# Kernel tuning notes

Hardware: AMD Instinct MI355X
Metric: run time of the kernel (lower is better)

## Reference

```python
import jax, jax.numpy as jnp
import numpy as np

H, T, E = 8, 2048, 512


def setup_inputs() -> dict:
    key = jax.random.key(0)
    ks = jax.random.split(key, 11)
    s_e = 1.0 / np.sqrt(E)
    s_f = 1.0 / np.sqrt(H * T)
    return {
        "x": jax.random.normal(ks[0], (T, E), jnp.float32),
        "y": jax.random.normal(ks[1], (T, E), jnp.float32),
        "z": jax.random.normal(ks[2], (T, E), jnp.float32),
        "Wq": jax.random.normal(ks[3], (H, E, E), jnp.float32) * s_e,
        "bq": jax.random.normal(ks[4], (H, E), jnp.float32) * s_e,
        "Wk": jax.random.normal(ks[5], (H, E, E), jnp.float32) * s_e,
        "bk": jax.random.normal(ks[6], (H, E), jnp.float32) * s_e,
        "Wv": jax.random.normal(ks[7], (H, E, E), jnp.float32) * s_e,
        "bv": jax.random.normal(ks[8], (H, E), jnp.float32) * s_e,
        "Wf": jax.random.normal(ks[9], (T, H * T), jnp.float32) * s_f,
        "bf": jax.random.normal(ks[10], (T,), jnp.float32) * s_f,
    }


def reference(x, y, z, Wq, bq, Wk, bk, Wv, bv, Wf, bf):
    # Per-head projections: torch Linear is x @ W.T + b, W is [out,in]
    q = jnp.einsum("se,hfe->hsf", x, Wq) + bq[:, None, :]  # [H,T,E]
    k = jnp.einsum("se,hfe->hsf", y, Wk) + bk[:, None, :]
    v = jnp.einsum("se,hfe->hsf", z, Wv) + bv[:, None, :]
    # Scores scaled by sqrt(num query rows) = sqrt(T), as in the source
    scores = jnp.einsum("hsf,htf->hst", q, k) / jnp.sqrt(jnp.asarray(T, x.dtype))
    att = jax.nn.softmax(scores, axis=-1)
    heads_out = jnp.einsum("hst,htf->hsf", att, v)  # [H,T,E]
    concat = heads_out.reshape(H * T, E)  # cat along dim 0
    # finalLinear applied to concat.T: [E, H*T] @ Wf.T -> [E, T], then transpose
    final = (concat.T @ Wf.T + bf).T  # [T, E]
    residual = final + z
    # Manual per-row LayerNorm: (x - mean) / sqrt(std^2 + 1e-4), population std
    mean = jnp.mean(residual, axis=1, keepdims=True)
    var = jnp.var(residual, axis=1, keepdims=True)
    return (residual - mean) / jnp.sqrt(var + 1e-4)
```

## Files before the change

### kernel.cpp

```cpp
#include <hip/hip_runtime.h>
#include <hip/hip_bf16.h>
#include <cstdint>


#define HH 8
#define TT 2048
#define EE 512
#define HT (HH * TT)

typedef __bf16 bf16_t;
typedef __attribute__((ext_vector_type(8))) __bf16 bf16x8;
typedef __attribute__((ext_vector_type(4))) float f32x4;

__device__ __forceinline__ void stage_half(const bf16_t* __restrict__ g, bf16_t* l) {
  __builtin_amdgcn_global_load_lds(
      (const __attribute__((address_space(1))) unsigned int*)g,
      (__attribute__((address_space(3))) unsigned int*)l, 16, 0, 0);
}
__device__ __forceinline__ void stage_half(const float* __restrict__ g, bf16_t* l) {
  float4 u = ((const float4*)g)[0];
  float4 v = ((const float4*)g)[1];
  bf16x8 o;
  o[0] = (__bf16)u.x; o[1] = (__bf16)u.y; o[2] = (__bf16)u.z; o[3] = (__bf16)u.w;
  o[4] = (__bf16)v.x; o[5] = (__bf16)v.y; o[6] = (__bf16)v.z; o[7] = (__bf16)v.w;
  *(bf16x8*)l = o;
}

template <typename CT, bool ATOMIC>
__device__ __forceinline__ void store_c(CT* p, float v) {
  if constexpr (ATOMIC) atomicAdd((float*)p, v);
  else *p = (CT)v;
}

template <typename AT, typename CT, bool ATOMIC>
__global__ __launch_bounds__(256) void mfma_gemm_nt(
    const AT* __restrict__ A, const bf16_t* __restrict__ B, CT* __restrict__ C,
    const float* __restrict__ bias_m, const float* __restrict__ bias_n,
    int K, int lda, int ldb, int ldc,
    int64_t sA, int64_t sB, int64_t sC, int64_t sBM, int64_t sBN) {
  const int z = blockIdx.z;
  A += z * sA;
  B += z * sB;
  C += z * sC;
  if (bias_m) bias_m += z * sBM;
  if (bias_n) bias_n += z * sBN;

  const int m0 = blockIdx.x * 128;
  const int n0 = blockIdx.y * 128;
  const int tid = threadIdx.x;

  __shared__ bf16_t sAb[128 * 32];
  __shared__ bf16_t sBb[128 * 32];

  const int srow = tid >> 2;
  const int scol = (tid & 3) * 8;
  const AT* a0 = A + (int64_t)(m0 + srow) * lda + scol;
  const AT* a1 = a0 + (int64_t)64 * lda;
  const bf16_t* b0 = B + (int64_t)(n0 + srow) * ldb + scol;
  const bf16_t* b1 = b0 + (int64_t)64 * ldb;
  bf16_t* la0 = sAb + tid * 8;
  bf16_t* la1 = sAb + 2048 + tid * 8;
  bf16_t* lb0 = sBb + tid * 8;
  bf16_t* lb1 = sBb + 2048 + tid * 8;

  const int wave = tid >> 6;
  const int lane = tid & 63;
  const int wm = (wave >> 1) * 64;
  const int wn = (wave & 1) * 64;
  const int fr = lane & 15;
  const int qd = lane >> 4;

  f32x4 acc[4][4];
#pragma unroll
  for (int i = 0; i < 4; i++)
#pragma unroll
    for (int j = 0; j < 4; j++) acc[i][j] = (f32x4){0.f, 0.f, 0.f, 0.f};

  for (int kt = 0; kt < K; kt += 32) {
    __syncthreads();
    stage_half(a0 + kt, la0);
    stage_half(a1 + kt, la1);
    stage_half(b0 + kt, lb0);
    stage_half(b1 + kt, lb1);
    __syncthreads();

    bf16x8 af[4], bf_[4];
#pragma unroll
    for (int i = 0; i < 4; i++)
      af[i] = *(const bf16x8*)&sAb[(wm + i * 16 + fr) * 32 + qd * 8];
#pragma unroll
    for (int j = 0; j < 4; j++)
      bf_[j] = *(const bf16x8*)&sBb[(wn + j * 16 + fr) * 32 + qd * 8];
#pragma unroll
    for (int i = 0; i < 4; i++)
#pragma unroll
      for (int j = 0; j < 4; j++)
        acc[i][j] = __builtin_amdgcn_mfma_f32_16x16x32_bf16(af[i], bf_[j], acc[i][j], 0, 0, 0);
  }

#pragma unroll
  for (int i = 0; i < 4; i++) {
    const int row0 = m0 + wm + i * 16 + qd * 4;
#pragma unroll
    for (int j = 0; j < 4; j++) {
      const int col = n0 + wn + j * 16 + fr;
      const float bn = bias_n ? bias_n[col] : 0.f;
#pragma unroll
      for (int r = 0; r < 4; r++) {
        const float bm = bias_m ? bias_m[row0 + r] : 0.f;
        store_c<CT, ATOMIC>(&C[(int64_t)(row0 + r) * ldc + col], acc[i][j][r] + bn + bm);
      }
    }
  }
}

__global__ __launch_bounds__(256) void cvt_bf16(const float* __restrict__ s,
                                                bf16_t* __restrict__ d) {
  const int64_t i = ((int64_t)blockIdx.x * 256 + threadIdx.x) * 8;
  float4 u = ((const float4*)(s + i))[0];
  float4 v = ((const float4*)(s + i))[1];
  bf16x8 o;
  o[0] = (__bf16)u.x; o[1] = (__bf16)u.y; o[2] = (__bf16)u.z; o[3] = (__bf16)u.w;
  o[4] = (__bf16)v.x; o[5] = (__bf16)v.y; o[6] = (__bf16)v.z; o[7] = (__bf16)v.w;
  *(bf16x8*)(d + i) = o;
}

__global__ __launch_bounds__(256) void softmax_rows(bf16_t* __restrict__ S) {
  const float scale = 0.022097086912079608f;
  bf16_t* p = S + (int64_t)blockIdx.x * TT;
  const int tid = threadIdx.x;
  float v[8];
  float mx = -1e30f;
#pragma unroll
  for (int i = 0; i < 8; i++) {
    v[i] = (float)p[tid + i * 256] * scale;
    mx = fmaxf(mx, v[i]);
  }
#pragma unroll
  for (int o = 32; o > 0; o >>= 1) mx = fmaxf(mx, __shfl_xor(mx, o));
  __shared__ float redm[4], reds[4];
  if ((tid & 63) == 0) redm[tid >> 6] = mx;
  __syncthreads();
  mx = fmaxf(fmaxf(redm[0], redm[1]), fmaxf(redm[2], redm[3]));
  float sum = 0.f;
#pragma unroll
  for (int i = 0; i < 8; i++) {
    v[i] = __expf(v[i] - mx);
    sum += v[i];
  }
#pragma unroll
  for (int o = 32; o > 0; o >>= 1) sum += __shfl_xor(sum, o);
  if ((tid & 63) == 0) reds[tid >> 6] = sum;
  __syncthreads();
  sum = reds[0] + reds[1] + reds[2] + reds[3];
  const float inv = 1.0f / sum;
#pragma unroll
  for (int i = 0; i < 8; i++) p[tid + i * 256] = (__bf16)(v[i] * inv);
}

__global__ __launch_bounds__(256) void ln_res(const float* __restrict__ F,
                                              const float* __restrict__ Z,
                                              const float* __restrict__ BF,
                                              float* __restrict__ O) {
  const int row = blockIdx.x;
  const float* f = F + (int64_t)row * EE;
  const float* z = Z + (int64_t)row * EE;
  float* o = O + (int64_t)row * EE;
  const float bft = BF[row];
  const int tid = threadIdx.x;
  const float a = f[tid] + bft + z[tid];
  const float b = f[tid + 256] + bft + z[tid + 256];
  float s = a + b, ss = a * a + b * b;
#pragma unroll
  for (int w = 32; w > 0; w >>= 1) {
    s += __shfl_xor(s, w);
    ss += __shfl_xor(ss, w);
  }
  __shared__ float rs[4], rss[4];
  if ((tid & 63) == 0) {
    rs[tid >> 6] = s;
    rss[tid >> 6] = ss;
  }
  __syncthreads();
  s = rs[0] + rs[1] + rs[2] + rs[3];
  ss = rss[0] + rss[1] + rss[2] + rss[3];
  const float mean = s * (1.0f / EE);
  const float var = ss * (1.0f / EE) - mean * mean;
  const float inv = rsqrtf(var + 1e-4f);
  o[tid] = (a - mean) * inv;
  o[tid + 256] = (b - mean) * inv;
}

extern "C" void kernel_launch(void* const* d_in, const int* in_sizes, int n_in,
                              void* d_out, int out_size, void* d_ws, size_t ws_size,
                              hipStream_t stream) {
  const float* x = (const float*)d_in[0];
  const float* y = (const float*)d_in[1];
  const float* z = (const float*)d_in[2];
  const float* Wq = (const float*)d_in[3];
  const float* bq = (const float*)d_in[4];
  const float* Wk = (const float*)d_in[5];
  const float* bk = (const float*)d_in[6];
  const float* Wv = (const float*)d_in[7];
  const float* bv = (const float*)d_in[8];
  const float* Wf = (const float*)d_in[9];
  const float* bfb = (const float*)d_in[10];
  float* out = (float*)d_out;

  const size_t MB = 1ull << 20;
  char* p = (char*)d_ws;

  const int64_t nTE = (int64_t)TT * EE;
  const int64_t nW = (int64_t)HH * EE * EE;

  if (ws_size >= 151 * MB) {
    bf16_t* xb = (bf16_t*)(p + 0 * MB);
    bf16_t* yb = (bf16_t*)(p + 2 * MB);
    bf16_t* zb = (bf16_t*)(p + 4 * MB);
    bf16_t* Wqb = (bf16_t*)(p + 6 * MB);
    bf16_t* Wkb = (bf16_t*)(p + 10 * MB);
    bf16_t* Wvb = (bf16_t*)(p + 14 * MB);
    bf16_t* q = (bf16_t*)(p + 18 * MB);
    bf16_t* k = (bf16_t*)(p + 34 * MB);
    bf16_t* vT = (bf16_t*)(p + 50 * MB);
    bf16_t* att = (bf16_t*)(p + 66 * MB);
    bf16_t* hoT = (bf16_t*)(p + 130 * MB);
    float* fin = (float*)(p + 146 * MB);

    cvt_bf16<<<nTE / 2048, 256, 0, stream>>>(x, xb);
    cvt_bf16<<<nTE / 2048, 256, 0, stream>>>(y, yb);
    cvt_bf16<<<nTE / 2048, 256, 0, stream>>>(z, zb);
    cvt_bf16<<<nW / 2048, 256, 0, stream>>>(Wq, Wqb);
    cvt_bf16<<<nW / 2048, 256, 0, stream>>>(Wk, Wkb);
    cvt_bf16<<<nW / 2048, 256, 0, stream>>>(Wv, Wvb);

    mfma_gemm_nt<bf16_t, bf16_t, false><<<dim3(16, 4, 8), 256, 0, stream>>>(
        xb, Wqb, q, nullptr, bq, EE, EE, EE, EE, 0, (int64_t)EE * EE, (int64_t)TT * EE, 0, EE);
    mfma_gemm_nt<bf16_t, bf16_t, false><<<dim3(16, 4, 8), 256, 0, stream>>>(
        yb, Wkb, k, nullptr, bk, EE, EE, EE, EE, 0, (int64_t)EE * EE, (int64_t)TT * EE, 0, EE);
    mfma_gemm_nt<bf16_t, bf16_t, false><<<dim3(4, 16, 8), 256, 0, stream>>>(
        Wvb, zb, vT, bv, nullptr, EE, EE, EE, TT, (int64_t)EE * EE, 0, (int64_t)EE * TT, EE, 0);
    mfma_gemm_nt<bf16_t, bf16_t, false><<<dim3(16, 16, 8), 256, 0, stream>>>(
        q, k, att, nullptr, nullptr, EE, EE, EE, TT, (int64_t)TT * EE, (int64_t)TT * EE,
        (int64_t)TT * TT, 0, 0);
    softmax_rows<<<HH * TT, 256, 0, stream>>>(att);
    mfma_gemm_nt<bf16_t, bf16_t, false><<<dim3(4, 16, 8), 256, 0, stream>>>(
        vT, att, hoT, nullptr, nullptr, TT, TT, TT, HT, (int64_t)EE * TT, (int64_t)TT * TT,
        (int64_t)TT, 0, 0);
    hipMemsetAsync(fin, 0, (size_t)TT * EE * 4, stream);
    mfma_gemm_nt<float, float, true><<<dim3(16, 4, 8), 256, 0, stream>>>(
        Wf, hoT, fin, nullptr, nullptr, HT / 8, HT, HT, EE, HT / 8, HT / 8, 0, 0, 0);
    ln_res<<<TT, 256, 0, stream>>>(fin, z, bfb, out);
  } else {
    bf16_t* xb = (bf16_t*)(p + 0 * MB);
    bf16_t* yb = (bf16_t*)(p + 2 * MB);
    bf16_t* zb = (bf16_t*)(p + 4 * MB);
    bf16_t* Wqb = (bf16_t*)(p + 6 * MB);
    bf16_t* Wkb = (bf16_t*)(p + 10 * MB);
    bf16_t* Wvb = (bf16_t*)(p + 14 * MB);
    bf16_t* qh = (bf16_t*)(p + 18 * MB);
    bf16_t* kh = (bf16_t*)(p + 20 * MB);
    bf16_t* vTh = (bf16_t*)(p + 22 * MB);
    bf16_t* att = (bf16_t*)(p + 24 * MB);
    bf16_t* hoT = (bf16_t*)(p + 32 * MB);
    float* fin = (float*)(p + 48 * MB);

    cvt_bf16<<<nTE / 2048, 256, 0, stream>>>(x, xb);
    cvt_bf16<<<nTE / 2048, 256, 0, stream>>>(y, yb);
    cvt_bf16<<<nTE / 2048, 256, 0, stream>>>(z, zb);
    cvt_bf16<<<nW / 2048, 256, 0, stream>>>(Wq, Wqb);
    cvt_bf16<<<nW / 2048, 256, 0, stream>>>(Wk, Wkb);
    cvt_bf16<<<nW / 2048, 256, 0, stream>>>(Wv, Wvb);

    for (int h = 0; h < HH; h++) {
      const bf16_t* Wq_h = Wqb + (int64_t)h * EE * EE;
      const bf16_t* Wk_h = Wkb + (int64_t)h * EE * EE;
      const bf16_t* Wv_h = Wvb + (int64_t)h * EE * EE;
      mfma_gemm_nt<bf16_t, bf16_t, false><<<dim3(16, 4, 1), 256, 0, stream>>>(
          xb, Wq_h, qh, nullptr, bq + h * EE, EE, EE, EE, EE, 0, 0, 0, 0, 0);
      mfma_gemm_nt<bf16_t, bf16_t, false><<<dim3(16, 4, 1), 256, 0, stream>>>(
          yb, Wk_h, kh, nullptr, bk + h * EE, EE, EE, EE, EE, 0, 0, 0, 0, 0);
      mfma_gemm_nt<bf16_t, bf16_t, false><<<dim3(4, 16, 1), 256, 0, stream>>>(
          Wv_h, zb, vTh, bv + h * EE, nullptr, EE, EE, EE, TT, 0, 0, 0, 0, 0);
      mfma_gemm_nt<bf16_t, bf16_t, false><<<dim3(16, 16, 1), 256, 0, stream>>>(
          qh, kh, att, nullptr, nullptr, EE, EE, EE, TT, 0, 0, 0, 0, 0);
      softmax_rows<<<TT, 256, 0, stream>>>(att);
      mfma_gemm_nt<bf16_t, bf16_t, false><<<dim3(4, 16, 1), 256, 0, stream>>>(
          vTh, att, hoT + (int64_t)h * TT, nullptr, nullptr, TT, TT, TT, HT, 0, 0, 0, 0, 0);
    }
    hipMemsetAsync(fin, 0, (size_t)TT * EE * 4, stream);
    mfma_gemm_nt<float, float, true><<<dim3(16, 4, 8), 256, 0, stream>>>(
        Wf, hoT, fin, nullptr, nullptr, HT / 8, HT, HT, EE, HT / 8, HT / 8, 0, 0, 0);
    ln_res<<<TT, 256, 0, stream>>>(fin, z, bfb, out);
  }
}
```

Before: 528.6 us.

## Add split-K for PV and final GEMMs, fp32 register prefetch, vectorized softmax

The GEMM kernel gains a templated split-K dimension (NZK) folded into blockIdx.z; bias is added only by the first K slice. It also gains register prefetch of the next fp32 tile, so global loads overlap with the MFMA loop. When the workspace is large enough, a new path splits the attention-times-V GEMM in two, accumulating into a zero-initialised fp32 hoT buffer with atomics. The final Wf GEMM is split 16 ways on every path, and softmax loads and stores rows with contiguous 16-byte vectors. The aim is more parallelism and better latency hiding, at the cost of extra memsets, atomic traffic and a larger fp32 intermediate.

```diff
diff --git a/kernel.cpp b/kernel.cpp
--- a/kernel.cpp
+++ b/kernel.cpp
@@ -1,6 +1,7 @@
 #include <hip/hip_runtime.h>
 #include <hip/hip_bf16.h>
 #include <cstdint>
+#include <type_traits>
 
 
 #define HH 8
@@ -12,17 +13,21 @@
 typedef __attribute__((ext_vector_type(8))) __bf16 bf16x8;
 typedef __attribute__((ext_vector_type(4))) float f32x4;
 
-__device__ __forceinline__ void stage_half(const bf16_t* __restrict__ g, bf16_t* l) {
+__device__ __forceinline__ void stage_lds(const bf16_t* __restrict__ g, bf16_t* l) {
   __builtin_amdgcn_global_load_lds(
       (const __attribute__((address_space(1))) unsigned int*)g,
       (__attribute__((address_space(3))) unsigned int*)l, 16, 0, 0);
 }
-__device__ __forceinline__ void stage_half(const float* __restrict__ g, bf16_t* l) {
-  float4 u = ((const float4*)g)[0];
-  float4 v = ((const float4*)g)[1];
+
+struct PF { float4 lo, hi; };
+__device__ __forceinline__ void pf_load(const float* __restrict__ g, PF& r) {
+  r.lo = ((const float4*)g)[0];
+  r.hi = ((const float4*)g)[1];
+}
+__device__ __forceinline__ void pf_store(bf16_t* l, const PF& r) {
   bf16x8 o;
-  o[0] = (__bf16)u.x; o[1] = (__bf16)u.y; o[2] = (__bf16)u.z; o[3] = (__bf16)u.w;
-  o[4] = (__bf16)v.x; o[5] = (__bf16)v.y; o[6] = (__bf16)v.z; o[7] = (__bf16)v.w;
+  o[0] = (__bf16)r.lo.x; o[1] = (__bf16)r.lo.y; o[2] = (__bf16)r.lo.z; o[3] = (__bf16)r.lo.w;
+  o[4] = (__bf16)r.hi.x; o[5] = (__bf16)r.hi.y; o[6] = (__bf16)r.hi.z; o[7] = (__bf16)r.hi.w;
   *(bf16x8*)l = o;
 }
 
@@ -32,18 +37,23 @@
   else *p = (CT)v;
 }
 
-template <typename AT, typename CT, bool ATOMIC>
+template <typename AT, typename BT, typename CT, bool ATOMIC, int NZK>
 __global__ __launch_bounds__(256) void mfma_gemm_nt(
-    const AT* __restrict__ A, const bf16_t* __restrict__ B, CT* __restrict__ C,
+    const AT* __restrict__ A, const BT* __restrict__ B, CT* __restrict__ C,
     const float* __restrict__ bias_m, const float* __restrict__ bias_n,
     int K, int lda, int ldb, int ldc,
-    int64_t sA, int64_t sB, int64_t sC, int64_t sBM, int64_t sBN) {
-  const int z = blockIdx.z;
-  A += z * sA;
-  B += z * sB;
-  C += z * sC;
-  if (bias_m) bias_m += z * sBM;
-  if (bias_n) bias_n += z * sBN;
+    int64_t sAh, int64_t sAk, int64_t sBh, int64_t sBk, int64_t sCh,
+    int64_t sBMh, int64_t sBNh) {
+  constexpr bool A_F32 = std::is_same<AT, float>::value;
+  constexpr bool B_F32 = std::is_same<BT, float>::value;
+  const int zh = blockIdx.z / NZK;
+  const int zk = blockIdx.z % NZK;
+  A += zh * sAh + zk * sAk;
+  B += zh * sBh + zk * sBk;
+  C += zh * sCh;
+  const bool do_bias = (zk == 0);
+  if (bias_m) bias_m += zh * sBMh;
+  if (bias_n) bias_n += zh * sBNh;
 
   const int m0 = blockIdx.x * 128;
   const int n0 = blockIdx.y * 128;
@@ -56,8 +66,8 @@
   const int scol = (tid & 3) * 8;
   const AT* a0 = A + (int64_t)(m0 + srow) * lda + scol;
   const AT* a1 = a0 + (int64_t)64 * lda;
-  const bf16_t* b0 = B + (int64_t)(n0 + srow) * ldb + scol;
-  const bf16_t* b1 = b0 + (int64_t)64 * ldb;
+  const BT* b0 = B + (int64_t)(n0 + srow) * ldb + scol;
+  const BT* b1 = b0 + (int64_t)64 * ldb;
   bf16_t* la0 = sAb + tid * 8;
   bf16_t* la1 = sAb + 2048 + tid * 8;
   bf16_t* lb0 = sBb + tid * 8;
@@ -76,26 +86,50 @@
 #pragma unroll
     for (int j = 0; j < 4; j++) acc[i][j] = (f32x4){0.f, 0.f, 0.f, 0.f};
 
+  PF pa0, pa1, pb0, pb1;
+  if constexpr (A_F32) { pf_load((const float*)a0, pa0); pf_load((const float*)a1, pa1); }
+  if constexpr (B_F32) { pf_load((const float*)b0, pb0); pf_load((const float*)b1, pb1); }
+
   for (int kt = 0; kt < K; kt += 32) {
     __syncthreads();
-    stage_half(a0 + kt, la0);
-    stage_half(a1 + kt, la1);
-    stage_half(b0 + kt, lb0);
-    stage_half(b1 + kt, lb1);
+    if constexpr (A_F32) {
+      pf_store(la0, pa0);
+      pf_store(la1, pa1);
+    } else {
+      stage_lds((const bf16_t*)a0 + kt, la0);
+      stage_lds((const bf16_t*)a1 + kt, la1);
+    }
+    if constexpr (B_F32) {
+      pf_store(lb0, pb0);
+      pf_store(lb1, pb1);
+    } else {
+      stage_lds((const bf16_t*)b0 + kt, lb0);
+      stage_lds((const bf16_t*)b1 + kt, lb1);
+    }
+    if (kt + 32 < K) {
+      if constexpr (A_F32) {
+        pf_load((const float*)a0 + kt + 32, pa0);
+        pf_load((const float*)a1 + kt + 32, pa1);
+      }
+      if constexpr (B_F32) {
+        pf_load((const float*)b0 + kt + 32, pb0);
+        pf_load((const float*)b1 + kt + 32, pb1);
+      }
+    }
     __syncthreads();
 
-    bf16x8 af[4], bf_[4];
+    bf16x8 af[4], bfr[4];
 #pragma unroll
     for (int i = 0; i < 4; i++)
       af[i] = *(const bf16x8*)&sAb[(wm + i * 16 + fr) * 32 + qd * 8];
 #pragma unroll
     for (int j = 0; j < 4; j++)
-      bf_[j] = *(const bf16x8*)&sBb[(wn + j * 16 + fr) * 32 + qd * 8];
+      bfr[j] = *(const bf16x8*)&sBb[(wn + j * 16 + fr) * 32 + qd * 8];
 #pragma unroll
     for (int i = 0; i < 4; i++)
 #pragma unroll
       for (int j = 0; j < 4; j++)
-        acc[i][j] = __builtin_amdgcn_mfma_f32_16x16x32_bf16(af[i], bf_[j], acc[i][j], 0, 0, 0);
+        acc[i][j] = __builtin_amdgcn_mfma_f32_16x16x32_bf16(af[i], bfr[j], acc[i][j], 0, 0, 0);
   }
 
 #pragma unroll
@@ -104,10 +138,10 @@
 #pragma unroll
     for (int j = 0; j < 4; j++) {
       const int col = n0 + wn + j * 16 + fr;
-      const float bn = bias_n ? bias_n[col] : 0.f;
+      const float bn = (bias_n && do_bias) ? bias_n[col] : 0.f;
 #pragma unroll
       for (int r = 0; r < 4; r++) {
-        const float bm = bias_m ? bias_m[row0 + r] : 0.f;
+        const float bm = (bias_m && do_bias) ? bias_m[row0 + r] : 0.f;
         store_c<CT, ATOMIC>(&C[(int64_t)(row0 + r) * ldc + col], acc[i][j][r] + bn + bm);
       }
     }
@@ -129,11 +163,12 @@
   const float scale = 0.022097086912079608f;
   bf16_t* p = S + (int64_t)blockIdx.x * TT;
   const int tid = threadIdx.x;
+  bf16x8 rv = *(const bf16x8*)(p + tid * 8);
   float v[8];
   float mx = -1e30f;
 #pragma unroll
   for (int i = 0; i < 8; i++) {
-    v[i] = (float)p[tid + i * 256] * scale;
+    v[i] = (float)rv[i] * scale;
     mx = fmaxf(mx, v[i]);
   }
 #pragma unroll
@@ -154,8 +189,10 @@
   __syncthreads();
   sum = reds[0] + reds[1] + reds[2] + reds[3];
   const float inv = 1.0f / sum;
-#pragma unroll
-  for (int i = 0; i < 8; i++) p[tid + i * 256] = (__bf16)(v[i] * inv);
+  bf16x8 ov;
+#pragma unroll
+  for (int i = 0; i < 8; i++) ov[i] = (__bf16)(v[i] * inv);
+  *(bf16x8*)(p + tid * 8) = ov;
 }
 
 __global__ __launch_bounds__(256) void ln_res(const float* __restrict__ F,
@@ -209,17 +246,52 @@
 
   const size_t MB = 1ull << 20;
   char* p = (char*)d_ws;
-
   const int64_t nTE = (int64_t)TT * EE;
   const int64_t nW = (int64_t)HH * EE * EE;
 
-  if (ws_size >= 151 * MB) {
-    bf16_t* xb = (bf16_t*)(p + 0 * MB);
-    bf16_t* yb = (bf16_t*)(p + 2 * MB);
-    bf16_t* zb = (bf16_t*)(p + 4 * MB);
-    bf16_t* Wqb = (bf16_t*)(p + 6 * MB);
-    bf16_t* Wkb = (bf16_t*)(p + 10 * MB);
-    bf16_t* Wvb = (bf16_t*)(p + 14 * MB);
+  bf16_t* xb = (bf16_t*)(p + 0 * MB);
+  bf16_t* yb = (bf16_t*)(p + 2 * MB);
+  bf16_t* zb = (bf16_t*)(p + 4 * MB);
+  bf16_t* Wqb = (bf16_t*)(p + 6 * MB);
+  bf16_t* Wkb = (bf16_t*)(p + 10 * MB);
+  bf16_t* Wvb = (bf16_t*)(p + 14 * MB);
+  cvt_bf16<<<nTE / 2048, 256, 0, stream>>>(x, xb);
+  cvt_bf16<<<nTE / 2048, 256, 0, stream>>>(y, yb);
+  cvt_bf16<<<nTE / 2048, 256, 0, stream>>>(z, zb);
+  cvt_bf16<<<nW / 2048, 256, 0, stream>>>(Wq, Wqb);
+  cvt_bf16<<<nW / 2048, 256, 0, stream>>>(Wk, Wkb);
+  cvt_bf16<<<nW / 2048, 256, 0, stream>>>(Wv, Wvb);
+
+  if (ws_size >= 167 * MB) {
+    bf16_t* q = (bf16_t*)(p + 18 * MB);
+    bf16_t* k = (bf16_t*)(p + 34 * MB);
+    bf16_t* vT = (bf16_t*)(p + 50 * MB);
+    bf16_t* att = (bf16_t*)(p + 66 * MB);
+    float* hoT = (float*)(p + 130 * MB);
+    float* fin = (float*)(p + 162 * MB);
+
+    mfma_gemm_nt<bf16_t, bf16_t, bf16_t, false, 1><<<dim3(16, 4, 8), 256, 0, stream>>>(
+        xb, Wqb, q, nullptr, bq, EE, EE, EE, EE, 0, 0, (int64_t)EE * EE, 0,
+        (int64_t)TT * EE, 0, EE);
+    mfma_gemm_nt<bf16_t, bf16_t, bf16_t, false, 1><<<dim3(16, 4, 8), 256, 0, stream>>>(
+        yb, Wkb, k, nullptr, bk, EE, EE, EE, EE, 0, 0, (int64_t)EE * EE, 0,
+        (int64_t)TT * EE, 0, EE);
+    mfma_gemm_nt<bf16_t, bf16_t, bf16_t, false, 1><<<dim3(4, 16, 8), 256, 0, stream>>>(
+        Wvb, zb, vT, bv, nullptr, EE, EE, EE, TT, (int64_t)EE * EE, 0, 0, 0,
+        (int64_t)EE * TT, EE, 0);
+    mfma_gemm_nt<bf16_t, bf16_t, bf16_t, false, 1><<<dim3(16, 16, 8), 256, 0, stream>>>(
+        q, k, att, nullptr, nullptr, EE, EE, EE, TT, (int64_t)TT * EE, 0,
+        (int64_t)TT * EE, 0, (int64_t)TT * TT, 0, 0);
+    softmax_rows<<<HH * TT, 256, 0, stream>>>(att);
+    hipMemsetAsync(hoT, 0, (size_t)EE * HT * 4, stream);
+    mfma_gemm_nt<bf16_t, bf16_t, float, true, 2><<<dim3(4, 16, 16), 256, 0, stream>>>(
+        vT, att, hoT, nullptr, nullptr, 1024, TT, TT, HT, (int64_t)EE * TT, 1024,
+        (int64_t)TT * TT, 1024, TT, 0, 0);
+    hipMemsetAsync(fin, 0, (size_t)TT * EE * 4, stream);
+    mfma_gemm_nt<float, float, float, true, 16><<<dim3(16, 4, 16), 256, 0, stream>>>(
+        Wf, hoT, fin, nullptr, nullptr, 1024, HT, HT, EE, 0, 1024, 0, 1024, 0, 0, 0);
+    ln_res<<<TT, 256, 0, stream>>>(fin, z, bfb, out);
+  } else if (ws_size >= 151 * MB) {
     bf16_t* q = (bf16_t*)(p + 18 * MB);
     bf16_t* k = (bf16_t*)(p + 34 * MB);
     bf16_t* vT = (bf16_t*)(p + 50 * MB);
@@ -227,37 +299,27 @@
     bf16_t* hoT = (bf16_t*)(p + 130 * MB);
     float* fin = (float*)(p + 146 * MB);
 
-    cvt_bf16<<<nTE / 2048, 256, 0, stream>>>(x, xb);
-    cvt_bf16<<<nTE / 2048, 256, 0, stream>>>(y, yb);
-    cvt_bf16<<<nTE / 2048, 256, 0, stream>>>(z, zb);
-    cvt_bf16<<<nW / 2048, 256, 0, stream>>>(Wq, Wqb);
-    cvt_bf16<<<nW / 2048, 256, 0, stream>>>(Wk, Wkb);
-    cvt_bf16<<<nW / 2048, 256, 0, stream>>>(Wv, Wvb);
-
-    mfma_gemm_nt<bf16_t, bf16_t, false><<<dim3(16, 4, 8), 256, 0, stream>>>(
-        xb, Wqb, q, nullptr, bq, EE, EE, EE, EE, 0, (int64_t)EE * EE, (int64_t)TT * EE, 0, EE);
-    mfma_gemm_nt<bf16_t, bf16_t, false><<<dim3(16, 4, 8), 256, 0, stream>>>(
-        yb, Wkb, k, nullptr, bk, EE, EE, EE, EE, 0, (int64_t)EE * EE, (int64_t)TT * EE, 0, EE);
-    mfma_gemm_nt<bf16_t, bf16_t, false><<<dim3(4, 16, 8), 256, 0, stream>>>(
-        Wvb, zb, vT, bv, nullptr, EE, EE, EE, TT, (int64_t)EE * EE, 0, (int64_t)EE * TT, EE, 0);
-    mfma_gemm_nt<bf16_t, bf16_t, false><<<dim3(16, 16, 8), 256, 0, stream>>>(
-        q, k, att, nullptr, nullptr, EE, EE, EE, TT, (int64_t)TT * EE, (int64_t)TT * EE,
-        (int64_t)TT * TT, 0, 0);
+    mfma_gemm_nt<bf16_t, bf16_t, bf16_t, false, 1><<<dim3(16, 4, 8), 256, 0, stream>>>(
+        xb, Wqb, q, nullptr, bq, EE, EE, EE, EE, 0, 0, (int64_t)EE * EE, 0,
+        (int64_t)TT * EE, 0, EE);
+    mfma_gemm_nt<bf16_t, bf16_t, bf16_t, false, 1><<<dim3(16, 4, 8), 256, 0, stream>>>(
+        yb, Wkb, k, nullptr, bk, EE, EE, EE, EE, 0, 0, (int64_t)EE * EE, 0,
+        (int64_t)TT * EE, 0, EE);
+    mfma_gemm_nt<bf16_t, bf16_t, bf16_t, false, 1><<<dim3(4, 16, 8), 256, 0, stream>>>(
+        Wvb, zb, vT, bv, nullptr, EE, EE, EE, TT, (int64_t)EE * EE, 0, 0, 0,
+        (int64_t)EE * TT, EE, 0);
+    mfma_gemm_nt<bf16_t, bf16_t, bf16_t, false, 1><<<dim3(16, 16, 8), 256, 0, stream>>>(
+        q, k, att, nullptr, nullptr, EE, EE, EE, TT, (int64_t)TT * EE, 0,
+        (int64_t)TT * EE, 0, (int64_t)TT * TT, 0, 0);
     softmax_rows<<<HH * TT, 256, 0, stream>>>(att);
-    mfma_gemm_nt<bf16_t, bf16_t, false><<<dim3(4, 16, 8), 256, 0, stream>>>(
-        vT, att, hoT, nullptr, nullptr, TT, TT, TT, HT, (int64_t)EE * TT, (int64_t)TT * TT,
-        (int64_t)TT, 0, 0);
+    mfma_gemm_nt<bf16_t, bf16_t, bf16_t, false, 1><<<dim3(4, 16, 8), 256, 0, stream>>>(
+        vT, att, hoT, nullptr, nullptr, TT, TT, TT, HT, (int64_t)EE * TT, 0,
+        (int64_t)TT * TT, 0, TT, 0, 0);
     hipMemsetAsync(fin, 0, (size_t)TT * EE * 4, stream);
-    mfma_gemm_nt<float, float, true><<<dim3(16, 4, 8), 256, 0, stream>>>(
-        Wf, hoT, fin, nullptr, nullptr, HT / 8, HT, HT, EE, HT / 8, HT / 8, 0, 0, 0);
+    mfma_gemm_nt<float, bf16_t, float, true, 16><<<dim3(16, 4, 16), 256, 0, stream>>>(
+        Wf, hoT, fin, nullptr, nullptr, 1024, HT, HT, EE, 0, 1024, 0, 1024, 0, 0, 0);
     ln_res<<<TT, 256, 0, stream>>>(fin, z, bfb, out);
   } else {
-    bf16_t* xb = (bf16_t*)(p + 0 * MB);
-    bf16_t* yb = (bf16_t*)(p + 2 * MB);
-    bf16_t* zb = (bf16_t*)(p + 4 * MB);
-    bf16_t* Wqb = (bf16_t*)(p + 6 * MB);
-    bf16_t* Wkb = (bf16_t*)(p + 10 * MB);
-    bf16_t* Wvb = (bf16_t*)(p + 14 * MB);
     bf16_t* qh = (bf16_t*)(p + 18 * MB);
     bf16_t* kh = (bf16_t*)(p + 20 * MB);
     bf16_t* vTh = (bf16_t*)(p + 22 * MB);
@@ -265,32 +327,26 @@
     bf16_t* hoT = (bf16_t*)(p + 32 * MB);
     float* fin = (float*)(p + 48 * MB);
 
-    cvt_bf16<<<nTE / 2048, 256, 0, stream>>>(x, xb);
-    cvt_bf16<<<nTE / 2048, 256, 0, stream>>>(y, yb);
-    cvt_bf16<<<nTE / 2048, 256, 0, stream>>>(z, zb);
-    cvt_bf16<<<nW / 2048, 256, 0, stream>>>(Wq, Wqb);
-    cvt_bf16<<<nW / 2048, 256, 0, stream>>>(Wk, Wkb);
-    cvt_bf16<<<nW / 2048, 256, 0, stream>>>(Wv, Wvb);
-
     for (int h = 0; h < HH; h++) {
       const bf16_t* Wq_h = Wqb + (int64_t)h * EE * EE;
       const bf16_t* Wk_h = Wkb + (int64_t)h * EE * EE;
       const bf16_t* Wv_h = Wvb + (int64_t)h * EE * EE;
-      mfma_gemm_nt<bf16_t, bf16_t, false><<<dim3(16, 4, 1), 256, 0, stream>>>(
-          xb, Wq_h, qh, nullptr, bq + h * EE, EE, EE, EE, EE, 0, 0, 0, 0, 0);
-      mfma_gemm_nt<bf16_t, bf16_t, false><<<dim3(16, 4, 1), 256, 0, stream>>>(
-          yb, Wk_h, kh, nullptr, bk + h * EE, EE, EE, EE, EE, 0, 0, 0, 0, 0);
-      mfma_gemm_nt<bf16_t, bf16_t, false><<<dim3(4, 16, 1), 256, 0, stream>>>(
-          Wv_h, zb, vTh, bv + h * EE, nullptr, EE, EE, EE, TT, 0, 0, 0, 0, 0);
-      mfma_gemm_nt<bf16_t, bf16_t, false><<<dim3(16, 16, 1), 256, 0, stream>>>(
-          qh, kh, att, nullptr, nullptr, EE, EE, EE, TT, 0, 0, 0, 0, 0);
+      mfma_gemm_nt<bf16_t, bf16_t, bf16_t, false, 1><<<dim3(16, 4, 1), 256, 0, stream>>>(
+          xb, Wq_h, qh, nullptr, bq + h * EE, EE, EE, EE, EE, 0, 0, 0, 0, 0, 0, 0);
+      mfma_gemm_nt<bf16_t, bf16_t, bf16_t, false, 1><<<dim3(16, 4, 1), 256, 0, stream>>>(
+          yb, Wk_h, kh, nullptr, bk + h * EE, EE, EE, EE, EE, 0, 0, 0, 0, 0, 0, 0);
+      mfma_gemm_nt<bf16_t, bf16_t, bf16_t, false, 1><<<dim3(4, 16, 1), 256, 0, stream>>>(
+          Wv_h, zb, vTh, bv + h * EE, nullptr, EE, EE, EE, TT, 0, 0, 0, 0, 0, 0, 0);
+      mfma_gemm_nt<bf16_t, bf16_t, bf16_t, false, 1><<<dim3(16, 16, 1), 256, 0, stream>>>(
+          qh, kh, att, nullptr, nullptr, EE, EE, EE, TT, 0, 0, 0, 0, 0, 0, 0);
       softmax_rows<<<TT, 256, 0, stream>>>(att);
-      mfma_gemm_nt<bf16_t, bf16_t, false><<<dim3(4, 16, 1), 256, 0, stream>>>(
-          vTh, att, hoT + (int64_t)h * TT, nullptr, nullptr, TT, TT, TT, HT, 0, 0, 0, 0, 0);
+      mfma_gemm_nt<bf16_t, bf16_t, bf16_t, false, 1><<<dim3(4, 16, 1), 256, 0, stream>>>(
+          vTh, att, hoT + (int64_t)h * TT, nullptr, nullptr, TT, TT, TT, HT, 0, 0, 0, 0, 0,
+          0, 0);
     }
     hipMemsetAsync(fin, 0, (size_t)TT * EE * 4, stream);
-    mfma_gemm_nt<float, float, true><<<dim3(16, 4, 8), 256, 0, stream>>>(
-        Wf, hoT, fin, nullptr, nullptr, HT / 8, HT, HT, EE, HT / 8, HT / 8, 0, 0, 0);
+    mfma_gemm_nt<float, bf16_t, float, true, 16><<<dim3(16, 4, 16), 256, 0, stream>>>(
+        Wf, hoT, fin, nullptr, nullptr, 1024, HT, HT, EE, 0, 1024, 0, 1024, 0, 0, 0);
     ln_res<<<TT, 256, 0, stream>>>(fin, z, bfb, out);
   }
 }
```

Measured after the change: 593.4 us. 12.3% more time.

## Pre-convert Wf to bf16, replace atomic split-K with partial planes summed in LayerNorm

Applied to the files above, without the earlier changes.

The final projection previously read the fp32 Wf inside the GEMM, converting it on the fly, and combined eight split-K slices with atomicAdd into a zeroed buffer. Now Wf is converted to bf16 once by a separate kernel and loaded with direct global-to-LDS copies. The GEMM splits K four ways into separate fp32 planes, and the LayerNorm kernel sums those planes, which removes the memset and the atomics. Softmax also switches to vectorized 8-wide bf16 loads and stores, the small-workspace fallback path is dropped, and buffers are aliased (fin4 over q, Wfb over att), which requires the large workspace.

```diff
diff --git a/kernel.cpp b/kernel.cpp
--- a/kernel.cpp
+++ b/kernel.cpp
@@ -12,38 +12,24 @@
 typedef __attribute__((ext_vector_type(8))) __bf16 bf16x8;
 typedef __attribute__((ext_vector_type(4))) float f32x4;
 
-__device__ __forceinline__ void stage_half(const bf16_t* __restrict__ g, bf16_t* l) {
+__device__ __forceinline__ void stage_lds(const bf16_t* __restrict__ g, bf16_t* l) {
   __builtin_amdgcn_global_load_lds(
       (const __attribute__((address_space(1))) unsigned int*)g,
       (__attribute__((address_space(3))) unsigned int*)l, 16, 0, 0);
 }
-__device__ __forceinline__ void stage_half(const float* __restrict__ g, bf16_t* l) {
-  float4 u = ((const float4*)g)[0];
-  float4 v = ((const float4*)g)[1];
-  bf16x8 o;
-  o[0] = (__bf16)u.x; o[1] = (__bf16)u.y; o[2] = (__bf16)u.z; o[3] = (__bf16)u.w;
-  o[4] = (__bf16)v.x; o[5] = (__bf16)v.y; o[6] = (__bf16)v.z; o[7] = (__bf16)v.w;
-  *(bf16x8*)l = o;
-}
-
-template <typename CT, bool ATOMIC>
-__device__ __forceinline__ void store_c(CT* p, float v) {
-  if constexpr (ATOMIC) atomicAdd((float*)p, v);
-  else *p = (CT)v;
-}
-
-template <typename AT, typename CT, bool ATOMIC>
+
+template <typename CT>
 __global__ __launch_bounds__(256) void mfma_gemm_nt(
-    const AT* __restrict__ A, const bf16_t* __restrict__ B, CT* __restrict__ C,
+    const bf16_t* __restrict__ A, const bf16_t* __restrict__ B, CT* __restrict__ C,
     const float* __restrict__ bias_m, const float* __restrict__ bias_n,
     int K, int lda, int ldb, int ldc,
-    int64_t sA, int64_t sB, int64_t sC, int64_t sBM, int64_t sBN) {
+    int64_t sAz, int64_t sBz, int64_t sCz, int64_t sBMz, int64_t sBNz) {
   const int z = blockIdx.z;
-  A += z * sA;
-  B += z * sB;
-  C += z * sC;
-  if (bias_m) bias_m += z * sBM;
-  if (bias_n) bias_n += z * sBN;
+  A += z * sAz;
+  B += z * sBz;
+  C += z * sCz;
+  if (bias_m) bias_m += z * sBMz;
+  if (bias_n) bias_n += z * sBNz;
 
   const int m0 = blockIdx.x * 128;
   const int n0 = blockIdx.y * 128;
@@ -54,8 +40,8 @@
 
   const int srow = tid >> 2;
   const int scol = (tid & 3) * 8;
-  const AT* a0 = A + (int64_t)(m0 + srow) * lda + scol;
-  const AT* a1 = a0 + (int64_t)64 * lda;
+  const bf16_t* a0 = A + (int64_t)(m0 + srow) * lda + scol;
+  const bf16_t* a1 = a0 + (int64_t)64 * lda;
   const bf16_t* b0 = B + (int64_t)(n0 + srow) * ldb + scol;
   const bf16_t* b1 = b0 + (int64_t)64 * ldb;
   bf16_t* la0 = sAb + tid * 8;
@@ -78,24 +64,24 @@
 
   for (int kt = 0; kt < K; kt += 32) {
     __syncthreads();
-    stage_half(a0 + kt, la0);
-    stage_half(a1 + kt, la1);
-    stage_half(b0 + kt, lb0);
-    stage_half(b1 + kt, lb1);
+    stage_lds(a0 + kt, la0);
+    stage_lds(a1 + kt, la1);
+    stage_lds(b0 + kt, lb0);
+    stage_lds(b1 + kt, lb1);
     __syncthreads();
 
-    bf16x8 af[4], bf_[4];
+    bf16x8 af[4], bfr[4];
 #pragma unroll
     for (int i = 0; i < 4; i++)
       af[i] = *(const bf16x8*)&sAb[(wm + i * 16 + fr) * 32 + qd * 8];
 #pragma unroll
     for (int j = 0; j < 4; j++)
-      bf_[j] = *(const bf16x8*)&sBb[(wn + j * 16 + fr) * 32 + qd * 8];
+      bfr[j] = *(const bf16x8*)&sBb[(wn + j * 16 + fr) * 32 + qd * 8];
 #pragma unroll
     for (int i = 0; i < 4; i++)
 #pragma unroll
       for (int j = 0; j < 4; j++)
-        acc[i][j] = __builtin_amdgcn_mfma_f32_16x16x32_bf16(af[i], bf_[j], acc[i][j], 0, 0, 0);
+        acc[i][j] = __builtin_amdgcn_mfma_f32_16x16x32_bf16(af[i], bfr[j], acc[i][j], 0, 0, 0);
   }
 
 #pragma unroll
@@ -108,7 +94,7 @@
 #pragma unroll
       for (int r = 0; r < 4; r++) {
         const float bm = bias_m ? bias_m[row0 + r] : 0.f;
-        store_c<CT, ATOMIC>(&C[(int64_t)(row0 + r) * ldc + col], acc[i][j][r] + bn + bm);
+        C[(int64_t)(row0 + r) * ldc + col] = (CT)(acc[i][j][r] + bn + bm);
       }
     }
   }
@@ -129,11 +115,12 @@
   const float scale = 0.022097086912079608f;
   bf16_t* p = S + (int64_t)blockIdx.x * TT;
   const int tid = threadIdx.x;
+  bf16x8 rv = *(const bf16x8*)(p + tid * 8);
   float v[8];
   float mx = -1e30f;
 #pragma unroll
   for (int i = 0; i < 8; i++) {
-    v[i] = (float)p[tid + i * 256] * scale;
+    v[i] = (float)rv[i] * scale;
     mx = fmaxf(mx, v[i]);
   }
 #pragma unroll
@@ -154,22 +141,31 @@
   __syncthreads();
   sum = reds[0] + reds[1] + reds[2] + reds[3];
   const float inv = 1.0f / sum;
-#pragma unroll
-  for (int i = 0; i < 8; i++) p[tid + i * 256] = (__bf16)(v[i] * inv);
-}
-
-__global__ __launch_bounds__(256) void ln_res(const float* __restrict__ F,
-                                              const float* __restrict__ Z,
-                                              const float* __restrict__ BF,
-                                              float* __restrict__ O) {
+  bf16x8 ov;
+#pragma unroll
+  for (int i = 0; i < 8; i++) ov[i] = (__bf16)(v[i] * inv);
+  *(bf16x8*)(p + tid * 8) = ov;
+}
+
+__global__ __launch_bounds__(256) void ln_res4(const float* __restrict__ F,
+                                               const float* __restrict__ Z,
+                                               const float* __restrict__ BF,
+                                               float* __restrict__ O) {
   const int row = blockIdx.x;
-  const float* f = F + (int64_t)row * EE;
-  const float* z = Z + (int64_t)row * EE;
-  float* o = O + (int64_t)row * EE;
+  const int64_t off = (int64_t)row * EE;
+  const int64_t plane = (int64_t)TT * EE;
+  const float* z = Z + off;
+  float* o = O + off;
   const float bft = BF[row];
   const int tid = threadIdx.x;
-  const float a = f[tid] + bft + z[tid];
-  const float b = f[tid + 256] + bft + z[tid + 256];
+  float a = bft + z[tid];
+  float b = bft + z[tid + 256];
+#pragma unroll
+  for (int zk = 0; zk < 4; zk++) {
+    const float* f = F + zk * plane + off;
+    a += f[tid];
+    b += f[tid + 256];
+  }
   float s = a + b, ss = a * a + b * b;
 #pragma unroll
   for (int w = 32; w > 0; w >>= 1) {
@@ -209,88 +205,46 @@
 
   const size_t MB = 1ull << 20;
   char* p = (char*)d_ws;
-
   const int64_t nTE = (int64_t)TT * EE;
   const int64_t nW = (int64_t)HH * EE * EE;
-
-  if (ws_size >= 151 * MB) {
-    bf16_t* xb = (bf16_t*)(p + 0 * MB);
-    bf16_t* yb = (bf16_t*)(p + 2 * MB);
-    bf16_t* zb = (bf16_t*)(p + 4 * MB);
-    bf16_t* Wqb = (bf16_t*)(p + 6 * MB);
-    bf16_t* Wkb = (bf16_t*)(p + 10 * MB);
-    bf16_t* Wvb = (bf16_t*)(p + 14 * MB);
-    bf16_t* q = (bf16_t*)(p + 18 * MB);
-    bf16_t* k = (bf16_t*)(p + 34 * MB);
-    bf16_t* vT = (bf16_t*)(p + 50 * MB);
-    bf16_t* att = (bf16_t*)(p + 66 * MB);
-    bf16_t* hoT = (bf16_t*)(p + 130 * MB);
-    float* fin = (float*)(p + 146 * MB);
-
-    cvt_bf16<<<nTE / 2048, 256, 0, stream>>>(x, xb);
-    cvt_bf16<<<nTE / 2048, 256, 0, stream>>>(y, yb);
-    cvt_bf16<<<nTE / 2048, 256, 0, stream>>>(z, zb);
-    cvt_bf16<<<nW / 2048, 256, 0, stream>>>(Wq, Wqb);
-    cvt_bf16<<<nW / 2048, 256, 0, stream>>>(Wk, Wkb);
-    cvt_bf16<<<nW / 2048, 256, 0, stream>>>(Wv, Wvb);
-
-    mfma_gemm_nt<bf16_t, bf16_t, false><<<dim3(16, 4, 8), 256, 0, stream>>>(
-        xb, Wqb, q, nullptr, bq, EE, EE, EE, EE, 0, (int64_t)EE * EE, (int64_t)TT * EE, 0, EE);
-    mfma_gemm_nt<bf16_t, bf16_t, false><<<dim3(16, 4, 8), 256, 0, stream>>>(
-        yb, Wkb, k, nullptr, bk, EE, EE, EE, EE, 0, (int64_t)EE * EE, (int64_t)TT * EE, 0, EE);
-    mfma_gemm_nt<bf16_t, bf16_t, false><<<dim3(4, 16, 8), 256, 0, stream>>>(
-        Wvb, zb, vT, bv, nullptr, EE, EE, EE, TT, (int64_t)EE * EE, 0, (int64_t)EE * TT, EE, 0);
-    mfma_gemm_nt<bf16_t, bf16_t, false><<<dim3(16, 16, 8), 256, 0, stream>>>(
-        q, k, att, nullptr, nullptr, EE, EE, EE, TT, (int64_t)TT * EE, (int64_t)TT * EE,
-        (int64_t)TT * TT, 0, 0);
-    softmax_rows<<<HH * TT, 256, 0, stream>>>(att);
-    mfma_gemm_nt<bf16_t, bf16_t, false><<<dim3(4, 16, 8), 256, 0, stream>>>(
-        vT, att, hoT, nullptr, nullptr, TT, TT, TT, HT, (int64_t)EE * TT, (int64_t)TT * TT,
-        (int64_t)TT, 0, 0);
-    hipMemsetAsync(fin, 0, (size_t)TT * EE * 4, stream);
-    mfma_gemm_nt<float, float, true><<<dim3(16, 4, 8), 256, 0, stream>>>(
-        Wf, hoT, fin, nullptr, nullptr, HT / 8, HT, HT, EE, HT / 8, HT / 8, 0, 0, 0);
-    ln_res<<<TT, 256, 0, stream>>>(fin, z, bfb, out);
-  } else {
-    bf16_t* xb = (bf16_t*)(p + 0 * MB);
-    bf16_t* yb = (bf16_t*)(p + 2 * MB);
-    bf16_t* zb = (bf16_t*)(p + 4 * MB);
-    bf16_t* Wqb = (bf16_t*)(p + 6 * MB);
-    bf16_t* Wkb = (bf16_t*)(p + 10 * MB);
-    bf16_t* Wvb = (bf16_t*)(p + 14 * MB);
-    bf16_t* qh = (bf16_t*)(p + 18 * MB);
-    bf16_t* kh = (bf16_t*)(p + 20 * MB);
-    bf16_t* vTh = (bf16_t*)(p + 22 * MB);
-    bf16_t* att = (bf16_t*)(p + 24 * MB);
-    bf16_t* hoT = (bf16_t*)(p + 32 * MB);
-    float* fin = (float*)(p + 48 * MB);
-
-    cvt_bf16<<<nTE / 2048, 256, 0, stream>>>(x, xb);
-    cvt_bf16<<<nTE / 2048, 256, 0, stream>>>(y, yb);
-    cvt_bf16<<<nTE / 2048, 256, 0, stream>>>(z, zb);
-    cvt_bf16<<<nW / 2048, 256, 0, stream>>>(Wq, Wqb);
-    cvt_bf16<<<nW / 2048, 256, 0, stream>>>(Wk, Wkb);
-    cvt_bf16<<<nW / 2048, 256, 0, stream>>>(Wv, Wvb);
-
-    for (int h = 0; h < HH; h++) {
-      const bf16_t* Wq_h = Wqb + (int64_t)h * EE * EE;
-      const bf16_t* Wk_h = Wkb + (int64_t)h * EE * EE;
-      const bf16_t* Wv_h = Wvb + (int64_t)h * EE * EE;
-      mfma_gemm_nt<bf16_t, bf16_t, false><<<dim3(16, 4, 1), 256, 0, stream>>>(
-          xb, Wq_h, qh, nullptr, bq + h * EE, EE, EE, EE, EE, 0, 0, 0, 0, 0);
-      mfma_gemm_nt<bf16_t, bf16_t, false><<<dim3(16, 4, 1), 256, 0, stream>>>(
-          yb, Wk_h, kh, nullptr, bk + h * EE, EE, EE, EE, EE, 0, 0, 0, 0, 0);
-      mfma_gemm_nt<bf16_t, bf16_t, false><<<dim3(4, 16, 1), 256, 0, stream>>>(
-          Wv_h, zb, vTh, bv + h * EE, nullptr, EE, EE, EE, TT, 0, 0, 0, 0, 0);
-      mfma_gemm_nt<bf16_t, bf16_t, false><<<dim3(16, 16, 1), 256, 0, stream>>>(
-          qh, kh, att, nullptr, nullptr, EE, EE, EE, TT, 0, 0, 0, 0, 0);
-      softmax_rows<<<TT, 256, 0, stream>>>(att);
-      mfma_gemm_nt<bf16_t, bf16_t, false><<<dim3(4, 16, 1), 256, 0, stream>>>(
-          vTh, att, hoT + (int64_t)h * TT, nullptr, nullptr, TT, TT, TT, HT, 0, 0, 0, 0, 0);
-    }
-    hipMemsetAsync(fin, 0, (size_t)TT * EE * 4, stream);
-    mfma_gemm_nt<float, float, true><<<dim3(16, 4, 8), 256, 0, stream>>>(
-        Wf, hoT, fin, nullptr, nullptr, HT / 8, HT, HT, EE, HT / 8, HT / 8, 0, 0, 0);
-    ln_res<<<TT, 256, 0, stream>>>(fin, z, bfb, out);
-  }
-}
+  const int64_t nWf = (int64_t)TT * HT;
+
+  bf16_t* xb = (bf16_t*)(p + 0 * MB);
+  bf16_t* yb = (bf16_t*)(p + 2 * MB);
+  bf16_t* zb = (bf16_t*)(p + 4 * MB);
+  bf16_t* Wqb = (bf16_t*)(p + 6 * MB);
+  bf16_t* Wkb = (bf16_t*)(p + 10 * MB);
+  bf16_t* Wvb = (bf16_t*)(p + 14 * MB);
+  bf16_t* q = (bf16_t*)(p + 18 * MB);
+  float* fin4 = (float*)(p + 18 * MB);
+  bf16_t* k = (bf16_t*)(p + 34 * MB);
+  bf16_t* vT = (bf16_t*)(p + 50 * MB);
+  bf16_t* att = (bf16_t*)(p + 66 * MB);
+  bf16_t* Wfb = (bf16_t*)(p + 66 * MB);
+  bf16_t* hoT = (bf16_t*)(p + 130 * MB);
+
+  cvt_bf16<<<nTE / 2048, 256, 0, stream>>>(x, xb);
+  cvt_bf16<<<nTE / 2048, 256, 0, stream>>>(y, yb);
+  cvt_bf16<<<nTE / 2048, 256, 0, stream>>>(z, zb);
+  cvt_bf16<<<nW / 2048, 256, 0, stream>>>(Wq, Wqb);
+  cvt_bf16<<<nW / 2048, 256, 0, stream>>>(Wk, Wkb);
+  cvt_bf16<<<nW / 2048, 256, 0, stream>>>(Wv, Wvb);
+
+  mfma_gemm_nt<bf16_t><<<dim3(16, 4, 8), 256, 0, stream>>>(
+      xb, Wqb, q, nullptr, bq, EE, EE, EE, EE, 0, (int64_t)EE * EE, (int64_t)TT * EE, 0, EE);
+  mfma_gemm_nt<bf16_t><<<dim3(16, 4, 8), 256, 0, stream>>>(
+      yb, Wkb, k, nullptr, bk, EE, EE, EE, EE, 0, (int64_t)EE * EE, (int64_t)TT * EE, 0, EE);
+  mfma_gemm_nt<bf16_t><<<dim3(4, 16, 8), 256, 0, stream>>>(
+      Wvb, zb, vT, bv, nullptr, EE, EE, EE, TT, (int64_t)EE * EE, 0, (int64_t)EE * TT, EE, 0);
+  mfma_gemm_nt<bf16_t><<<dim3(16, 16, 8), 256, 0, stream>>>(
+      q, k, att, nullptr, nullptr, EE, EE, EE, TT, (int64_t)TT * EE, (int64_t)TT * EE,
+      (int64_t)TT * TT, 0, 0);
+  softmax_rows<<<HH * TT, 256, 0, stream>>>(att);
+  mfma_gemm_nt<bf16_t><<<dim3(4, 16, 8), 256, 0, stream>>>(
+      vT, att, hoT, nullptr, nullptr, TT, TT, TT, HT, (int64_t)EE * TT, (int64_t)TT * TT,
+      (int64_t)TT, 0, 0);
+  cvt_bf16<<<nWf / 2048, 256, 0, stream>>>(Wf, Wfb);
+  mfma_gemm_nt<float><<<dim3(16, 4, 4), 256, 0, stream>>>(
+      Wfb, hoT, fin4, nullptr, nullptr, 4096, HT, HT, EE, 4096, 4096, (int64_t)TT * EE, 0, 0);
+  ln_res4<<<TT, 256, 0, stream>>>(fin4, z, bfb, out);
+}
```

Result: slower. 570.9 us (+8.0%).
